# Kernel tuning notes

Hardware: AMD Instinct MI355X
Metric: run time of the kernel (lower is better)

The kernel has to match this reference:

```python
import jax, jax.numpy as jnp
import numpy as np

C = 128      # in = out channels
H = 4        # heads
HD = C // H  # head dim
N_DRUG, N_DIS, E = 50000, 20000, 250000
EA_DIM = 8


def _seg_softmax(logits, seg, n):
    # torch_geometric.utils.softmax: per-destination-node softmax over incident edges
    m = jax.ops.segment_max(logits, seg, num_segments=n)          # [n,H]
    ex = jnp.exp(logits - m[seg])
    s = jax.ops.segment_sum(ex, seg, num_segments=n)
    return ex / (s[seg] + 1e-16)


def _edge_conv(src_x, dst_x, si, di, Ws, bs, Wd, bd, attn, gate, n_dst):
    msg_src = src_x[si] @ Ws + bs           # [E,C] gather + linear
    msg_dst = dst_x[di] @ Wd + bd
    msg = msg_src + msg_dst
    if gate is not None:
        msg = msg * gate
    e = msg.shape[0]
    mh = msg.reshape(e, H, HD)
    sh = msg_src.reshape(e, H, HD)
    dh = msg_dst.reshape(e, H, HD)
    logits = (sh * dh).sum(-1) / jnp.sqrt(jnp.float32(HD)) + (mh * attn).sum(-1)  # [E,H]
    w = _seg_softmax(logits, di, n_dst)
    out = (mh * w[..., None]).reshape(e, C)
    return jax.ops.segment_sum(out, di, num_segments=n_dst)      # [n_dst,C]


def setup_inputs() -> dict:
    key = jax.random.key(0)
    ks = jax.random.split(key, 24)
    s = 1.0 / np.sqrt(C)
    d = {
        'x_drug': jax.random.normal(ks[0], (N_DRUG, C), jnp.float32),
        'x_disease': jax.random.normal(ks[1], (N_DIS, C), jnp.float32),
        'ea_treats': jax.random.normal(ks[2], (E, EA_DIM), jnp.float32),
        'si_t': jax.random.randint(ks[3], (E,), 0, N_DRUG),
        'di_t': jax.random.randint(ks[4], (E,), 0, N_DIS),
        'si_r': jax.random.randint(ks[5], (E,), 0, N_DIS),
        'di_r': jax.random.randint(ks[6], (E,), 0, N_DRUG),
        'Ws_t': jax.random.normal(ks[7], (C, C), jnp.float32) * s,
        'bs_t': jnp.zeros((C,), jnp.float32),
        'Wd_t': jax.random.normal(ks[8], (C, C), jnp.float32) * s,
        'bd_t': jnp.zeros((C,), jnp.float32),
        'attn_t': jax.random.normal(ks[9], (1, H, HD), jnp.float32) * 0.1,
        'Wg1': jax.random.normal(ks[10], (EA_DIM, C), jnp.float32) * (1.0 / np.sqrt(EA_DIM)),
        'bg1': jnp.zeros((C,), jnp.float32),
        'Wg2': jax.random.normal(ks[11], (C, C), jnp.float32) * s,
        'bg2': jnp.zeros((C,), jnp.float32),
        'Ws_r': jax.random.normal(ks[12], (C, C), jnp.float32) * s,
        'bs_r': jnp.zeros((C,), jnp.float32),
        'Wd_r': jax.random.normal(ks[13], (C, C), jnp.float32) * s,
        'bd_r': jnp.zeros((C,), jnp.float32),
        'attn_r': jax.random.normal(ks[14], (1, H, HD), jnp.float32) * 0.1,
        'Wo_drug': jax.random.normal(ks[15], (C, C), jnp.float32) * s,
        'bo_drug': jnp.zeros((C,), jnp.float32),
        'Wo_dis': jax.random.normal(ks[16], (C, C), jnp.float32) * s,
        'bo_dis': jnp.zeros((C,), jnp.float32),
    }
    return d


def reference(x_drug, x_disease, ea_treats, si_t, di_t, si_r, di_r,
              Ws_t, bs_t, Wd_t, bd_t, attn_t, Wg1, bg1, Wg2, bg2,
              Ws_r, bs_r, Wd_r, bd_r, attn_r,
              Wo_drug, bo_drug, Wo_dis, bo_dis):
    # edge gate for (drug, treats, disease): continuous edge attrs -> Linear-GELU-Linear-Sigmoid
    gate = jax.nn.sigmoid(jax.nn.gelu(ea_treats @ Wg1 + bg1, approximate=False) @ Wg2 + bg2)
    aggr_dis = _edge_conv(x_drug, x_disease, si_t, di_t, Ws_t, bs_t, Wd_t, bd_t, attn_t, gate, N_DIS)
    aggr_drug = _edge_conv(x_disease, x_drug, si_r, di_r, Ws_r, bs_r, Wd_r, bd_r, attn_r, None, N_DRUG)
    # single message per node type -> mean is identity; then per-node-type lin_out
    out_drug = aggr_drug @ Wo_drug + bo_drug
    out_dis = aggr_dis @ Wo_dis + bo_dis
    return out_drug, out_dis
```

## Files before the change

### kernel.cpp

```cpp
#include <hip/hip_runtime.h>
#include <hip/hip_bf16.h>
#include <math.h>

#define N_DRUG 50000
#define N_DIS  20000
#define NE     250000
#define NE_PAD 250048

#define NB0 79
#define NBT 275

typedef __bf16 bf16x8 __attribute__((ext_vector_type(8)));
typedef __bf16 bf16x4 __attribute__((ext_vector_type(4)));
typedef __bf16 bf16x2 __attribute__((ext_vector_type(2)));
typedef float  f32x4  __attribute__((ext_vector_type(4)));
typedef float  f32x2  __attribute__((ext_vector_type(2)));

__device__ __forceinline__ bf16x8 bz8() {
  bf16x8 v;
  #pragma unroll
  for (int j = 0; j < 8; ++j) v[j] = (__bf16)0.f;
  return v;
}

__device__ __forceinline__ float gelu_fast(float x) {
  float ax = fabsf(x);
  float t = fmaf(ax, 0.019527f, 3.43654e-4f);
  t = fmaf(ax, t, 0.1151945f);
  t = fmaf(ax, t, 0.1968564f);
  float p = fmaf(ax, t, 1.0f);
  float p2 = p * p;
  float p4 = p2 * p2;
  float r = __builtin_amdgcn_rcpf(p4);
  float sel = (x >= 0.f) ? (2.0f - r) : r;
  return 0.5f * x * sel;
}

__device__ __forceinline__ float sigmoid_fast(float v) {
  return __builtin_amdgcn_rcpf(1.0f + __expf(-v));
}

template <int N>
__device__ __forceinline__ float dpp_ror(float v) {
  int r = __builtin_amdgcn_update_dpp(0, __builtin_bit_cast(int, v),
                                      0x120 | N, 0xF, 0xF, false);
  return __builtin_bit_cast(float, r);
}

struct Seg {
  const void* A[4];
  const float* W[4];
  const float* bias[4];
  void* out[4];
  int M[4];
  int bstart[5];
};

template <int AIN_BF16, int OUT_BF16>
__global__ __launch_bounds__(256)
void gemm_seg(Seg d)
{
  __shared__ __bf16 Wt[128][136];

  const int b = blockIdx.x;
  const int sidx = (b >= d.bstart[3]) ? 3 : (b >= d.bstart[2]) ? 2
                 : (b >= d.bstart[1]) ? 1 : 0;
  const int nb = d.bstart[sidx + 1] - d.bstart[sidx];
  const int lb = b - d.bstart[sidx];
  const float* W = d.W[sidx];
  const float* bias = d.bias[sidx];
  const int M = d.M[sidx];
  const int ntiles = (M + 63) >> 6;
  const int tid = threadIdx.x;
  const int wv = tid >> 6, lane = tid & 63;
  const int m16 = lane & 15, quad = lane >> 4;

  for (int idx = tid; idx < 16384; idx += 256) {
    int k = idx >> 7, n = idx & 127;
    Wt[n][k] = (__bf16)W[idx];
  }
  __syncthreads();

  float bv[8];
  #pragma unroll
  for (int ct = 0; ct < 8; ++ct) bv[ct] = bias[ct * 16 + m16];

  auto load_afr = [&](int t, bf16x8* afr) {
    const int arow = (t << 6) + wv * 16 + m16;
    const bool ok = (t < ntiles) && (arow < M);
    if (AIN_BF16) {
      const __bf16* ap = (const __bf16*)d.A[sidx] + (long)arow * 128 + quad * 8;
      #pragma unroll
      for (int kt = 0; kt < 4; ++kt)
        afr[kt] = ok ? *(const bf16x8*)(ap + kt * 32) : bz8();
    } else {
      const float* ap = (const float*)d.A[sidx] + (long)arow * 128 + quad * 8;
      #pragma unroll
      for (int kt = 0; kt < 4; ++kt) {
        bf16x8 v = bz8();
        if (ok) {
          f32x4 lo = *(const f32x4*)(ap + kt * 32);
          f32x4 hi = *(const f32x4*)(ap + kt * 32 + 4);
          #pragma unroll
          for (int j = 0; j < 4; ++j) { v[j] = (__bf16)lo[j]; v[4 + j] = (__bf16)hi[j]; }
        }
        afr[kt] = v;
      }
    }
  };

  bf16x8 afr[4];
  if (lb < ntiles) load_afr(lb, afr);

  for (int t = lb; t < ntiles; t += nb) {
    bf16x8 nafr[4];
    load_afr(t + nb, nafr);

    f32x4 acc[8];
    #pragma unroll
    for (int ct = 0; ct < 8; ++ct) acc[ct] = (f32x4){0.f, 0.f, 0.f, 0.f};
    #pragma unroll
    for (int kt = 0; kt < 4; ++kt) {
      #pragma unroll
      for (int ct = 0; ct < 8; ++ct) {
        bf16x8 bfr = *(const bf16x8*)&Wt[ct * 16 + m16][kt * 32 + quad * 8];
        acc[ct] = __builtin_amdgcn_mfma_f32_16x16x32_bf16(afr[kt], bfr, acc[ct], 0, 0, 0);
      }
    }

    const int rb = (t << 6) + wv * 16 + quad * 4;
    #pragma unroll
    for (int ct = 0; ct < 8; ++ct) {
      const int col = ct * 16 + m16;
      #pragma unroll
      for (int rg = 0; rg < 4; ++rg) {
        int gr = rb + rg;
        if (gr < M) {
          float v = acc[ct][rg] + bv[ct];
          if (OUT_BF16) ((__bf16*)d.out[sidx])[(long)gr * 128 + col] = (__bf16)v;
          else          ((float*)d.out[sidx])[(long)gr * 128 + col] = v;
        }
      }
    }
    #pragma unroll
    for (int kt = 0; kt < 4; ++kt) afr[kt] = nafr[kt];
  }
}

__global__ __launch_bounds__(256)
void gate_kernel(const float* __restrict__ W2,
                 const float* __restrict__ Wg1, const float* __restrict__ bg1,
                 const float* __restrict__ bg2,
                 __bf16* __restrict__ out)
{
  __shared__ __bf16 Wt[128][136];
  __shared__ __bf16 H[64][136];
  const int tid = threadIdx.x;
  const int wv = tid >> 6, lane = tid & 63;
  const int m16 = lane & 15, quad = lane >> 4;

  for (int idx = tid; idx < 16384; idx += 256) {
    int k = idx >> 7, n = idx & 127;
    Wt[n][k] = (__bf16)W2[idx];
  }
  __syncthreads();

  bf16x8 b1[8];
  #pragma unroll
  for (int ct = 0; ct < 8; ++ct) {
    bf16x8 v = bz8();
    if (quad == 0) {
      #pragma unroll
      for (int j = 0; j < 8; ++j) v[j] = (__bf16)Wg1[j * 128 + ct * 16 + m16];
    }
    b1[ct] = v;
  }
  float b1v[8], b2v[8];
  #pragma unroll
  for (int ct = 0; ct < 8; ++ct) {
    b1v[ct] = bg1[ct * 16 + m16];
    b2v[ct] = bg2[ct * 16 + m16];
  }

  const int ntiles = (NE + 63) >> 6;
  const int hr = wv * 16 + quad * 4;
  const int ar = wv * 16 + m16;

  for (int t = blockIdx.x; t < ntiles; t += gridDim.x) {
    const int p = (t << 6) + wv * 16 + m16;

    bf16x8 a1 = bz8();
    if (quad == 0)
      a1 = *(const bf16x8*)(out + (long)p * 128);

    f32x4 h[8];
    #pragma unroll
    for (int ct = 0; ct < 8; ++ct)
      h[ct] = __builtin_amdgcn_mfma_f32_16x16x32_bf16(a1, b1[ct], (f32x4){0.f,0.f,0.f,0.f}, 0, 0, 0);

    #pragma unroll
    for (int ct = 0; ct < 8; ++ct) {
      const int col = ct * 16 + m16;
      #pragma unroll
      for (int rg = 0; rg < 4; ++rg)
        H[hr + rg][col] = (__bf16)gelu_fast(h[ct][rg] + b1v[ct]);
    }
    asm volatile("s_waitcnt lgkmcnt(0)" ::: "memory");

    bf16x8 afr[4];
    #pragma unroll
    for (int kt = 0; kt < 4; ++kt)
      afr[kt] = *(const bf16x8*)&H[ar][kt * 32 + quad * 8];
    asm volatile("" ::: "memory");

    f32x4 acc[8];
    #pragma unroll
    for (int ct = 0; ct < 8; ++ct) acc[ct] = (f32x4){0.f, 0.f, 0.f, 0.f};
    #pragma unroll
    for (int kt = 0; kt < 4; ++kt) {
      #pragma unroll
      for (int ct = 0; ct < 8; ++ct) {
        bf16x8 bfr = *(const bf16x8*)&Wt[ct * 16 + m16][kt * 32 + quad * 8];
        acc[ct] = __builtin_amdgcn_mfma_f32_16x16x32_bf16(afr[kt], bfr, acc[ct], 0, 0, 0);
      }
    }

    #pragma unroll
    for (int ct = 0; ct < 8; ++ct) {
      const int col = ct * 16 + m16;
      #pragma unroll
      for (int rg = 0; rg < 4; ++rg)
        H[hr + rg][col] = (__bf16)sigmoid_fast(acc[ct][rg] + b2v[ct]);
    }
    asm volatile("s_waitcnt lgkmcnt(0)" ::: "memory");

    bf16x8 gout[4];
    #pragma unroll
    for (int kt = 0; kt < 4; ++kt)
      gout[kt] = *(const bf16x8*)&H[ar][kt * 32 + quad * 8];
    asm volatile("" ::: "memory");

    __bf16* op = out + (long)p * 128 + quad * 8;
    #pragma unroll
    for (int kt = 0; kt < 4; ++kt)
      *(bf16x8*)(op + kt * 32) = gout[kt];
  }
}

__global__ __launch_bounds__(256)
void histo2(const int* __restrict__ di_t, const int* __restrict__ di_r,
            int* __restrict__ cnt_dis, int* __restrict__ cnt_drug, int half) {
  int b = blockIdx.x;
  if (b < half) {
    int i = b * 256 + threadIdx.x;
    if (i < NE) atomicAdd(&cnt_dis[di_t[i]], 1);
  } else {
    int i = (b - half) * 256 + threadIdx.x;
    if (i < NE) atomicAdd(&cnt_drug[di_r[i]], 1);
  }
}

__global__ __launch_bounds__(256)
void scatter2(const int* __restrict__ di_t, const int* __restrict__ di_r,
              const int* __restrict__ si_t, const int* __restrict__ si_r,
              const float* __restrict__ EA,
              int* __restrict__ cur_dis, int* __restrict__ cur_drug,
              int* __restrict__ ssrc_t, int* __restrict__ ssrc_r,
              __bf16* __restrict__ gate_ea, int half) {
  int b = blockIdx.x;
  if (b < half) {
    int i = b * 256 + threadIdx.x;
    if (i < NE) {
      int p = atomicAdd(&cur_dis[di_t[i]], 1);
      ssrc_t[p] = si_t[i];
      f32x4 e0 = *(const f32x4*)(EA + (long)i * 8);
      f32x4 e1 = *(const f32x4*)(EA + (long)i * 8 + 4);
      bf16x8 v;
      #pragma unroll
      for (int j = 0; j < 4; ++j) { v[j] = (__bf16)e0[j]; v[4 + j] = (__bf16)e1[j]; }
      *(bf16x8*)(gate_ea + (long)p * 128) = v;
    }
    if (b == 0 && threadIdx.x < NE_PAD - NE) {
      *(bf16x8*)(gate_ea + (long)(NE + threadIdx.x) * 128) = bz8();
    }
  } else {
    int i = (b - half) * 256 + threadIdx.x;
    if (i < NE) {
      int p = atomicAdd(&cur_drug[di_r[i]], 1);
      ssrc_r[p] = si_r[i];
    }
  }
}

__device__ __forceinline__ void seg_geom(int b, int& base, int& n, int& lb) {
  if (b < NB0) { base = 0;     n = 20000; lb = b; }
  else         { base = 20000; n = 50000; lb = b - NB0; }
}

__global__ __launch_bounds__(256)
void scan_partial(const int* __restrict__ cnt, int* __restrict__ bsum) {
  __shared__ int sh[256];
  int b = blockIdx.x, t = threadIdx.x;
  int base, n, lb; seg_geom(b, base, n, lb);
  int i = lb * 256 + t;
  sh[t] = (i < n) ? cnt[base + i] : 0;
  __syncthreads();
  for (int d = 1; d < 256; d <<= 1) {
    int vv = (t >= d) ? sh[t - d] : 0;
    __syncthreads();
    sh[t] += vv;
    __syncthreads();
  }
  if (t == 255) bsum[b] = sh[255];
}

__global__ __launch_bounds__(512)
void scan_block(const int* __restrict__ bsum, int* __restrict__ bexc) {
  __shared__ int v[512];
  __shared__ int f[512];
  int t = threadIdx.x;
  int own = (t < NBT) ? bsum[t] : 0;
  v[t] = own;
  f[t] = (t == 0 || t == NB0 || t >= NBT) ? 1 : 0;
  __syncthreads();
  for (int d = 1; d < 512; d <<= 1) {
    int vv = 0, ff = 1;
    if (t >= d) { vv = v[t - d]; ff = f[t - d]; }
    __syncthreads();
    if (t >= d && !f[t]) { v[t] += vv; f[t] |= ff; }
    __syncthreads();
  }
  if (t < NBT) bexc[t] = v[t] - own;
}

__global__ __launch_bounds__(256)
void scan_final(const int* __restrict__ cnt, const int* __restrict__ bexc,
                int* __restrict__ offs, int* __restrict__ cursor) {
  __shared__ int sh[256];
  int b = blockIdx.x, t = threadIdx.x;
  int base, n, lb; seg_geom(b, base, n, lb);
  int i = lb * 256 + t;
  int own = (i < n) ? cnt[base + i] : 0;
  sh[t] = own;
  __syncthreads();
  for (int d = 1; d < 256; d <<= 1) {
    int vv = (t >= d) ? sh[t - d] : 0;
    __syncthreads();
    sh[t] += vv;
    __syncthreads();
  }
  int off = bexc[b] + sh[t] - own;
  if (i < n) { offs[base + i] = off; cursor[base + i] = off; }
}

__global__ __launch_bounds__(256)
void aggregate2(const __bf16* __restrict__ Xs_t, const __bf16* __restrict__ Xd_t,
                const __bf16* __restrict__ Xs_r, const __bf16* __restrict__ Xd_r,
                const int* __restrict__ ssrc_t, const int* __restrict__ ssrc_r,
                const int* __restrict__ offs, const int* __restrict__ cnt,
                const __bf16* __restrict__ gate_s,
                const float* __restrict__ attn_t, const float* __restrict__ attn_r,
                __bf16* __restrict__ aggr_dis, __bf16* __restrict__ aggr_drug)
{
  const int gw0 = (int)((blockIdx.x * 256 + threadIdx.x) >> 6);
  if (gw0 >= N_DIS + N_DRUG) return;
  const int gw = __builtin_amdgcn_readfirstlane(gw0);
  const int lane = threadIdx.x & 63;
  const int c = lane * 2;
  const bool isDis = gw < N_DIS;
  const int node = isDis ? gw : gw - N_DIS;
  const __bf16* __restrict__ Xs = isDis ? Xs_t : Xs_r;
  const __bf16* __restrict__ Xd = isDis ? Xd_t : Xd_r;
  const int* __restrict__ ssrc = isDis ? ssrc_t : ssrc_r;
  const float* __restrict__ attn = isDis ? attn_t : attn_r;
  __bf16* __restrict__ outp = isDis ? aggr_dis : aggr_drug;
  const int Ns = isDis ? N_DRUG : N_DIS;

  const int start = __builtin_amdgcn_readfirstlane(offs[gw]);
  const int m     = __builtin_amdgcn_readfirstlane(cnt[gw]);

  const float LOG2E = 1.4426950408889634f;
  f32x2 at = *(const f32x2*)(attn + c);
  bf16x2 xdb = *(const bf16x2*)(Xd + (size_t)node * 128 + c);
  const float xd0 = (float)xdb[0], xd1 = (float)xdb[1];
  const float xdl0 = xd0 * (0.17677669529663687f * LOG2E);
  const float xdl1 = xd1 * (0.17677669529663687f * LOG2E);
  const float at0 = at[0] * LOG2E, at1 = at[1] * LOG2E;

  auto sfetch = [&](int jn) -> int {
    int idx = start + jn;
    if (idx > NE - 1) idx = NE - 1;
    int s = __builtin_amdgcn_readfirstlane(ssrc[idx]);
    return ((unsigned)s < (unsigned)Ns) ? s : 0;
  };
  auto row_load = [&](int s) -> bf16x2 {
    return *(const bf16x2*)(Xs + (size_t)s * 128 + c);
  };
  auto gate_load = [&](int jn) -> bf16x2 {
    return *(const bf16x2*)(gate_s + (size_t)(start + jn) * 128 + c);
  };

  const bf16x2 z2 = {(__bf16)0.f, (__bf16)0.f};
  bf16x2 xa[4], ga[4], xb[4], gb[4];
  #pragma unroll
  for (int u = 0; u < 4; ++u) { xa[u] = z2; ga[u] = z2; xb[u] = z2; gb[u] = z2; }

  int s0[4], s1[4], s2[4];
  #pragma unroll
  for (int u = 0; u < 4; ++u) s0[u] = sfetch(u);
  #pragma unroll
  for (int u = 0; u < 4; ++u) s1[u] = sfetch(4 + u);
  #pragma unroll
  for (int u = 0; u < 4; ++u) s2[u] = sfetch(8 + u);

  #pragma unroll
  for (int u = 0; u < 4; ++u) {
    xa[u] = row_load(s0[u]);
    if (isDis) ga[u] = gate_load(u);
  }
  if (m > 4) {
    #pragma unroll
    for (int u = 0; u < 4; ++u) {
      xb[u] = row_load(s1[u]);
      if (isDis) gb[u] = gate_load(4 + u);
    }
  }

  float n0 = 0.f, n1 = 0.f, den = 0.f;

  for (int j = 0; j < m; j += 4) {
    bf16x2 xc[4], gc[4];
    #pragma unroll
    for (int u = 0; u < 4; ++u) { xc[u] = z2; gc[u] = z2; }
    if (j + 8 < m) {
      #pragma unroll
      for (int u = 0; u < 4; ++u) {
        xc[u] = row_load(s2[u]);
        if (isDis) gc[u] = gate_load(j + 8 + u);
      }
    }
    if (j + 12 < m) {
      #pragma unroll
      for (int u = 0; u < 4; ++u) s2[u] = sfetch(j + 12 + u);
    }

    float part[4], mm0[4], mm1[4];
    #pragma unroll
    for (int u = 0; u < 4; ++u) {
      float xs0 = (float)xa[u][0], xs1 = (float)xa[u][1];
      float m0 = xs0 + xd0, m1 = xs1 + xd1;
      if (isDis) { m0 *= (float)ga[u][0]; m1 *= (float)ga[u][1]; }
      mm0[u] = m0; mm1[u] = m1;
      part[u] = xs0 * xdl0 + xs1 * xdl1 + m0 * at0 + m1 * at1;
    }
    #pragma unroll
    for (int u = 0; u < 4; ++u) part[u] += dpp_ror<1>(part[u]);
    #pragma unroll
    for (int u = 0; u < 4; ++u) part[u] += dpp_ror<2>(part[u]);
    #pragma unroll
    for (int u = 0; u < 4; ++u) part[u] += dpp_ror<4>(part[u]);
    #pragma unroll
    for (int u = 0; u < 4; ++u) part[u] += dpp_ror<8>(part[u]);

    #pragma unroll
    for (int u = 0; u < 4; ++u) {
      float ex = (j + u < m) ? __builtin_amdgcn_exp2f(part[u]) : 0.f;
      n0 += mm0[u] * ex;
      n1 += mm1[u] * ex;
      den += ex;
    }
    #pragma unroll
    for (int u = 0; u < 4; ++u) {
      xa[u] = xb[u]; ga[u] = gb[u];
      xb[u] = xc[u]; gb[u] = gc[u];
    }
  }

  float r = __builtin_amdgcn_rcpf(den + 1e-16f);
  bf16x2 o;
  o[0] = (__bf16)(n0 * r);
  o[1] = (__bf16)(n1 * r);
  *(bf16x2*)(outp + (size_t)node * 128 + c) = o;
}

extern "C" void kernel_launch(void* const* d_in, const int* in_sizes, int n_in,
                              void* d_out, int out_size, void* d_ws, size_t ws_size,
                              hipStream_t stream)
{
  const float* x_drug  = (const float*)d_in[0];
  const float* x_dis   = (const float*)d_in[1];
  const float* ea      = (const float*)d_in[2];
  const int*   si_t    = (const int*)d_in[3];
  const int*   di_t    = (const int*)d_in[4];
  const int*   si_r    = (const int*)d_in[5];
  const int*   di_r    = (const int*)d_in[6];
  const float* Ws_t    = (const float*)d_in[7];
  const float* bs_t    = (const float*)d_in[8];
  const float* Wd_t    = (const float*)d_in[9];
  const float* bd_t    = (const float*)d_in[10];
  const float* attn_t  = (const float*)d_in[11];
  const float* Wg1     = (const float*)d_in[12];
  const float* bg1     = (const float*)d_in[13];
  const float* Wg2     = (const float*)d_in[14];
  const float* bg2     = (const float*)d_in[15];
  const float* Ws_r    = (const float*)d_in[16];
  const float* bs_r    = (const float*)d_in[17];
  const float* Wd_r    = (const float*)d_in[18];
  const float* bd_r    = (const float*)d_in[19];
  const float* attn_r  = (const float*)d_in[20];
  const float* Wo_drug = (const float*)d_in[21];
  const float* bo_drug = (const float*)d_in[22];
  const float* Wo_dis  = (const float*)d_in[23];
  const float* bo_dis  = (const float*)d_in[24];

  __bf16* wsb      = (__bf16*)d_ws;
  __bf16* Xs_t     = wsb;
  __bf16* Xd_t     = Xs_t + 6400000;
  __bf16* Xs_r     = Xd_t + 2560000;
  __bf16* Xd_r     = Xs_r + 2560000;
  __bf16* gate     = Xd_r + 6400000;
  int* cnt_dis    = (int*)(gate + (long)NE_PAD * 128);
  int* cnt_drug   = cnt_dis + 20000;
  int* offs_dis   = cnt_drug + 50000;
  int* offs_drug  = offs_dis + 20000;
  int* cur_dis    = offs_drug + 50000;
  int* cur_drug   = cur_dis + 20000;
  int* sorted_t   = cur_drug + 50000;
  int* ssrc_t     = sorted_t + 250000;
  int* ssrc_r     = ssrc_t + 250000;
  int* bsum       = ssrc_r + 250000;
  int* bexc       = bsum + 512;

  __bf16* aggr_dis  = Xd_t;
  __bf16* aggr_drug = Xd_r;

  float* out_drug = (float*)d_out;
  float* out_dis  = out_drug + (long)N_DRUG * 128;

  hipMemsetAsync(cnt_dis, 0, 70000 * sizeof(int), stream);

  const int eb = (NE + 255) / 256;

  histo2<<<2 * eb, 256, 0, stream>>>(di_t, di_r, cnt_dis, cnt_drug, eb);
  scan_partial<<<NBT, 256, 0, stream>>>(cnt_dis, bsum);
  scan_block<<<1, 512, 0, stream>>>(bsum, bexc);
  scan_final<<<NBT, 256, 0, stream>>>(cnt_dis, bexc, offs_dis, cur_dis);
  scatter2<<<2 * eb, 256, 0, stream>>>(di_t, di_r, si_t, si_r, ea,
                                       cur_dis, cur_drug, ssrc_t, ssrc_r,
                                       gate, eb);

  Seg nd;
  nd.A[0] = x_drug; nd.W[0] = Ws_t; nd.bias[0] = bs_t; nd.out[0] = Xs_t; nd.M[0] = N_DRUG;
  nd.A[1] = x_dis;  nd.W[1] = Wd_t; nd.bias[1] = bd_t; nd.out[1] = Xd_t; nd.M[1] = N_DIS;
  nd.A[2] = x_dis;  nd.W[2] = Ws_r; nd.bias[2] = bs_r; nd.out[2] = Xs_r; nd.M[2] = N_DIS;
  nd.A[3] = x_drug; nd.W[3] = Wd_r; nd.bias[3] = bd_r; nd.out[3] = Xd_r; nd.M[3] = N_DRUG;
  nd.bstart[0] = 0; nd.bstart[1] = 274; nd.bstart[2] = 384; nd.bstart[3] = 494; nd.bstart[4] = 768;
  gemm_seg<0, 1><<<768, 256, 0, stream>>>(nd);

  gate_kernel<<<768, 256, 0, stream>>>(Wg2, Wg1, bg1, bg2, gate);

  aggregate2<<<(N_DIS + N_DRUG + 3) / 4, 256, 0, stream>>>(
      Xs_t, Xd_t, Xs_r, Xd_r, ssrc_t, ssrc_r, offs_dis, cnt_dis,
      gate, attn_t, attn_r, aggr_dis, aggr_drug);

  Seg od;
  od.A[0] = aggr_drug; od.W[0] = Wo_drug; od.bias[0] = bo_drug; od.out[0] = out_drug; od.M[0] = N_DRUG;
  od.A[1] = aggr_dis;  od.W[1] = Wo_dis;  od.bias[1] = bo_dis;  od.out[1] = out_dis;  od.M[1] = N_DIS;
  od.A[2] = od.A[1];   od.W[2] = od.W[1]; od.bias[2] = od.bias[1]; od.out[2] = od.out[1]; od.M[2] = N_DIS;
  od.A[3] = od.A[1];   od.W[3] = od.W[1]; od.bias[3] = od.bias[1]; od.out[3] = od.out[1]; od.M[3] = N_DIS;
  od.bstart[0] = 0; od.bstart[1] = 548; od.bstart[2] = 768; od.bstart[3] = 768; od.bstart[4] = 768;
  gemm_seg<1, 0><<<768, 256, 0, stream>>>(od);
}
```

Before: 330.8 us.

## Fuse node-projection GEMM and edge-gate MLP into one interleaved launch

Merges the segmented node-feature GEMM and the edge gate MLP kernel into a single launch whose odd blocks run GEMM tiles and whose even blocks run gate tiles. Shared memory is carved manually so both paths reuse one buffer, and launch bounds request three blocks per CU. The aim is to drop one kernel launch and its tail gap, and to overlap the two independent workloads on the same CUs. In exchange, the gate path's larger shared-memory footprint now applies to GEMM blocks too, which may reduce occupancy for them.

After: 336.0 us. Within noise of the previous version (+1.5%).

```diff
diff --git a/kernel.cpp b/kernel.cpp
--- a/kernel.cpp
+++ b/kernel.cpp
@@ -57,12 +57,9 @@
 };
 
 template <int AIN_BF16, int OUT_BF16>
-__global__ __launch_bounds__(256)
-void gemm_seg(Seg d)
+__device__ __forceinline__ void gemm_seg_body(const Seg& d, int b,
+                                              __bf16 (*Wt)[136])
 {
-  __shared__ __bf16 Wt[128][136];
-
-  const int b = blockIdx.x;
   const int sidx = (b >= d.bstart[3]) ? 3 : (b >= d.bstart[2]) ? 2
                  : (b >= d.bstart[1]) ? 1 : 0;
   const int nb = d.bstart[sidx + 1] - d.bstart[sidx];
@@ -147,14 +144,22 @@
   }
 }
 
+template <int AIN_BF16, int OUT_BF16>
 __global__ __launch_bounds__(256)
-void gate_kernel(const float* __restrict__ W2,
-                 const float* __restrict__ Wg1, const float* __restrict__ bg1,
-                 const float* __restrict__ bg2,
-                 __bf16* __restrict__ out)
+void gemm_seg(Seg d)
 {
   __shared__ __bf16 Wt[128][136];
-  __shared__ __bf16 H[64][136];
+  gemm_seg_body<AIN_BF16, OUT_BF16>(d, blockIdx.x, Wt);
+}
+
+__device__ __forceinline__ void gate_body(const float* __restrict__ W2,
+                                          const float* __restrict__ Wg1,
+                                          const float* __restrict__ bg1,
+                                          const float* __restrict__ bg2,
+                                          __bf16* __restrict__ out,
+                                          int gb, int gstride,
+                                          __bf16 (*Wt)[136], __bf16 (*H)[136])
+{
   const int tid = threadIdx.x;
   const int wv = tid >> 6, lane = tid & 63;
   const int m16 = lane & 15, quad = lane >> 4;
@@ -186,7 +191,7 @@
   const int hr = wv * 16 + quad * 4;
   const int ar = wv * 16 + m16;
 
-  for (int t = blockIdx.x; t < ntiles; t += gridDim.x) {
+  for (int t = gb; t < ntiles; t += gstride) {
     const int p = (t << 6) + wv * 16 + m16;
 
     bf16x8 a1 = bz8();
@@ -244,6 +249,24 @@
     #pragma unroll
     for (int kt = 0; kt < 4; ++kt)
       *(bf16x8*)(op + kt * 32) = gout[kt];
+  }
+}
+
+__global__ __launch_bounds__(256, 3)
+void fused_nd_gate(Seg d,
+                   const float* __restrict__ W2, const float* __restrict__ Wg1,
+                   const float* __restrict__ bg1, const float* __restrict__ bg2,
+                   __bf16* __restrict__ gate_out)
+{
+  __shared__ __align__(16) char smem[52224];
+  __bf16 (*Wt)[136] = (__bf16 (*)[136])smem;
+  __bf16 (*H)[136]  = (__bf16 (*)[136])(smem + 34816);
+
+  const int vb = blockIdx.x >> 1;
+  if (blockIdx.x & 1) {
+    gemm_seg_body<0, 1>(d, vb, Wt);
+  } else {
+    gate_body(W2, Wg1, bg1, bg2, gate_out, vb, 768, Wt, H);
   }
 }
 
@@ -555,9 +578,7 @@
   nd.A[2] = x_dis;  nd.W[2] = Ws_r; nd.bias[2] = bs_r; nd.out[2] = Xs_r; nd.M[2] = N_DIS;
   nd.A[3] = x_drug; nd.W[3] = Wd_r; nd.bias[3] = bd_r; nd.out[3] = Xd_r; nd.M[3] = N_DRUG;
   nd.bstart[0] = 0; nd.bstart[1] = 274; nd.bstart[2] = 384; nd.bstart[3] = 494; nd.bstart[4] = 768;
-  gemm_seg<0, 1><<<768, 256, 0, stream>>>(nd);
-
-  gate_kernel<<<768, 256, 0, stream>>>(Wg2, Wg1, bg1, bg2, gate);
+  fused_nd_gate<<<1536, 256, 0, stream>>>(nd, Wg2, Wg1, bg1, bg2, gate);
 
   aggregate2<<<(N_DIS + N_DRUG + 3) / 4, 256, 0, stream>>>(
       Xs_t, Xd_t, Xs_r, Xd_r, ssrc_t, ssrc_r, offs_dis, cnt_dis,
```
